# Kernel optimization log

Measured on AMD Instinct MI355X. Metric: run time of the kernel, lower is better.

## Reference

```python
import jax, jax.numpy as jnp
import numpy as np

N_EMBD = 1024
N_HEAD = 16
HEAD_DIM = N_EMBD // N_HEAD
EPS = 1e-5


def _gelu_tanh(x):
    c = jnp.sqrt(jnp.asarray(2.0 / jnp.pi, x.dtype))
    return 0.5 * x * (1.0 + jnp.tanh(c * (x + 0.044715 * x ** 3)))


def _layernorm(x, scale, shift):
    # torch.var defaults to unbiased (ddof=1) -- replicate exactly
    mean = jnp.mean(x, axis=-1, keepdims=True)
    var = jnp.var(x, axis=-1, keepdims=True, ddof=1)
    return (x - mean) / jnp.sqrt(var + EPS) * scale + shift


def setup_inputs() -> dict:
    key = jax.random.key(0)
    ks = jax.random.split(key, 8)
    d, h = N_EMBD, 4 * N_EMBD
    s = 0.02
    return {
        "x": jax.random.normal(ks[0], (2, 2048, d), jnp.float32),
        "ln1_scale": jnp.ones((d,), jnp.float32),
        "ln1_shift": jnp.zeros((d,), jnp.float32),
        "wq": jax.random.normal(ks[1], (d, d), jnp.float32) * s,
        "wk": jax.random.normal(ks[2], (d, d), jnp.float32) * s,
        "wv": jax.random.normal(ks[3], (d, d), jnp.float32) * s,
        "w_out": jax.random.normal(ks[4], (d, d), jnp.float32) * s,
        "b_out": jnp.zeros((d,), jnp.float32),
        "ln2_scale": jnp.ones((d,), jnp.float32),
        "ln2_shift": jnp.zeros((d,), jnp.float32),
        "w1": jax.random.normal(ks[5], (d, h), jnp.float32) * s,
        "b1": jnp.zeros((h,), jnp.float32),
        "w2": jax.random.normal(ks[6], (h, d), jnp.float32) * s,
        "b2": jnp.zeros((d,), jnp.float32),
    }


def reference(x, ln1_scale, ln1_shift, wq, wk, wv, w_out, b_out,
              ln2_scale, ln2_shift, w1, b1, w2, b2):
    B, S, D = x.shape
    out = _layernorm(x, ln1_scale, ln1_shift)

    # qkv projections (no bias), split heads: [B, H, S, hd]
    q = (out @ wq).reshape(B, S, N_HEAD, HEAD_DIM).transpose(0, 2, 1, 3)
    k = (out @ wk).reshape(B, S, N_HEAD, HEAD_DIM).transpose(0, 2, 1, 3)
    v = (out @ wv).reshape(B, S, N_HEAD, HEAD_DIM).transpose(0, 2, 1, 3)

    scores = jnp.einsum("bhqd,bhkd->bhqk", q, k)
    causal = jnp.triu(jnp.ones((S, S), bool), k=1)
    # original masks BEFORE scaling; -inf / sqrt(d) is still -inf
    scores = jnp.where(causal, -jnp.inf, scores)
    weights = jax.nn.softmax(scores / jnp.sqrt(jnp.asarray(HEAD_DIM, scores.dtype)), axis=-1)
    ctx = jnp.einsum("bhqk,bhkd->bqhd", weights, v).reshape(B, S, D)
    attn_out = ctx @ w_out + b_out

    out = attn_out + x  # dropout is identity (rate 0)
    shortcut = out
    out = _layernorm(out, ln2_scale, ln2_shift)
    out = _gelu_tanh(out @ w1 + b1) @ w2 + b2
    return out + shortcut
```

## Files before the change

### kernel.cpp

```cpp
#include <hip/hip_runtime.h>
#include <stdint.h>
#include <math.h>

using bf16x8 = __attribute__((ext_vector_type(8))) short;
using f32x4  = __attribute__((ext_vector_type(4))) float;

__device__ __forceinline__ uint16_t f2b(float f) {
    union { float f; uint32_t i; } v; v.f = f;
    uint32_t r = v.i + 0x7fffu + ((v.i >> 16) & 1u);
    return (uint16_t)(r >> 16);
}
__device__ __forceinline__ float b2f(uint16_t u) {
    union { uint32_t i; float f; } v; v.i = ((uint32_t)u) << 16; return v.f;
}

typedef const __attribute__((address_space(1))) void gvoid;
typedef __attribute__((address_space(3))) void svoid;

__global__ __launch_bounds__(256) void fill_zero(float* __restrict__ o, int n) {
    int i = (blockIdx.x * 256 + threadIdx.x) * 4;
    if (i < n) *(float4*)(o + i) = make_float4(0.f, 0.f, 0.f, 0.f);
}

__global__ __launch_bounds__(256) void transpose_qkvo(
    const float* __restrict__ wq, const float* __restrict__ wk,
    const float* __restrict__ wv, const float* __restrict__ wo,
    uint16_t* __restrict__ wqkvT, uint16_t* __restrict__ woT)
{
    const int D = 1024;
    int z = blockIdx.z;
    const float* W = (z == 0) ? wq : (z == 1) ? wk : (z == 2) ? wv : wo;
    uint16_t* Wt = (z < 3) ? (wqkvT + (size_t)z * D * D) : woT;
    __shared__ uint16_t t[32][33];
    int n0 = blockIdx.x * 32, k0 = blockIdx.y * 32;
    int tx = threadIdx.x, ty = threadIdx.y;
    #pragma unroll
    for (int i = ty; i < 32; i += 8)
        t[i][tx] = f2b(W[(size_t)(k0 + i) * D + (n0 + tx)]);
    __syncthreads();
    #pragma unroll
    for (int i = ty; i < 32; i += 8)
        Wt[(size_t)(n0 + i) * D + (k0 + tx)] = t[tx][i];
}

__global__ __launch_bounds__(256) void transpose_f2b(
    const float* __restrict__ W, uint16_t* __restrict__ Wt, int K, int N)
{
    __shared__ uint16_t t[32][33];
    int n0 = blockIdx.x * 32, k0 = blockIdx.y * 32;
    int tx = threadIdx.x, ty = threadIdx.y;
    #pragma unroll
    for (int i = ty; i < 32; i += 8)
        t[i][tx] = f2b(W[(size_t)(k0 + i) * N + (n0 + tx)]);
    __syncthreads();
    #pragma unroll
    for (int i = ty; i < 32; i += 8)
        Wt[(size_t)(n0 + i) * K + (k0 + tx)] = t[tx][i];
}

__global__ __launch_bounds__(256) void ln_kernel(
    const float* __restrict__ src, const float* __restrict__ scale,
    const float* __restrict__ shift, uint16_t* __restrict__ out)
{
    const int D = 1024;
    int row = blockIdx.x, t = threadIdx.x;
    float4 f = *((const float4*)(src + (size_t)row * D) + t);
    float v[4] = {f.x, f.y, f.z, f.w};
    float s1 = v[0] + v[1] + v[2] + v[3];
    float s2 = v[0]*v[0] + v[1]*v[1] + v[2]*v[2] + v[3]*v[3];
    #pragma unroll
    for (int off = 32; off; off >>= 1) {
        s1 += __shfl_xor(s1, off);
        s2 += __shfl_xor(s2, off);
    }
    __shared__ float red[2][4];
    __shared__ float stat[2];
    int wid = t >> 6, lane = t & 63;
    if (lane == 0) { red[0][wid] = s1; red[1][wid] = s2; }
    __syncthreads();
    if (t == 0) {
        float S1 = red[0][0] + red[0][1] + red[0][2] + red[0][3];
        float S2 = red[1][0] + red[1][1] + red[1][2] + red[1][3];
        float mean = S1 / (float)D;
        float var  = fmaxf((S2 - mean * S1) / (float)(D - 1), 0.f);
        stat[0] = mean; stat[1] = rsqrtf(var + 1e-5f);
    }
    __syncthreads();
    float mean = stat[0], rstd = stat[1];
    float4 sc = *((const float4*)scale + t);
    float4 sh = *((const float4*)shift + t);
    uint16_t o[4];
    o[0] = f2b((v[0] - mean) * rstd * sc.x + sh.x);
    o[1] = f2b((v[1] - mean) * rstd * sc.y + sh.y);
    o[2] = f2b((v[2] - mean) * rstd * sc.z + sh.z);
    o[3] = f2b((v[3] - mean) * rstd * sc.w + sh.w);
    uint2 st;
    st.x = (uint32_t)o[0] | ((uint32_t)o[1] << 16);
    st.y = (uint32_t)o[2] | ((uint32_t)o[3] << 16);
    *(uint2*)(out + (size_t)row * D + t * 4) = st;
}

__global__ __launch_bounds__(256) void combine2(
    float* __restrict__ dst, const float* __restrict__ part0,
    const float* __restrict__ resid, const float* __restrict__ bias)
{
    const int D = 1024;
    size_t o = (size_t)blockIdx.x * D + threadIdx.x * 4;
    float4 a = *(float4*)(dst + o);
    float4 b = *(const float4*)(part0 + o);
    float4 c = *(const float4*)(resid + o);
    float4 bv = *((const float4*)bias + threadIdx.x);
    a.x += b.x + c.x + bv.x;
    a.y += b.y + c.y + bv.y;
    a.z += b.z + c.z + bv.z;
    a.w += b.w + c.w + bv.w;
    *(float4*)(dst + o) = a;
}

__global__ __launch_bounds__(256) void combine2ln(
    float* __restrict__ res1, const float* __restrict__ part0,
    const float* __restrict__ x, const float* __restrict__ bo,
    const float* __restrict__ scale, const float* __restrict__ shift,
    uint16_t* __restrict__ out)
{
    const int D = 1024;
    int row = blockIdx.x, t = threadIdx.x;
    size_t o = (size_t)row * D + t * 4;
    float4 a = *(float4*)(res1 + o);
    float4 b = *(const float4*)(part0 + o);
    float4 c = *(const float4*)(x + o);
    float4 bv = *((const float4*)bo + t);
    float v[4] = {a.x + b.x + c.x + bv.x, a.y + b.y + c.y + bv.y,
                  a.z + b.z + c.z + bv.z, a.w + b.w + c.w + bv.w};
    *(float4*)(res1 + o) = make_float4(v[0], v[1], v[2], v[3]);

    float s1 = v[0] + v[1] + v[2] + v[3];
    float s2 = v[0]*v[0] + v[1]*v[1] + v[2]*v[2] + v[3]*v[3];
    #pragma unroll
    for (int off = 32; off; off >>= 1) {
        s1 += __shfl_xor(s1, off);
        s2 += __shfl_xor(s2, off);
    }
    __shared__ float red[2][4];
    __shared__ float stat[2];
    int wid = t >> 6, lane = t & 63;
    if (lane == 0) { red[0][wid] = s1; red[1][wid] = s2; }
    __syncthreads();
    if (t == 0) {
        float S1 = red[0][0] + red[0][1] + red[0][2] + red[0][3];
        float S2 = red[1][0] + red[1][1] + red[1][2] + red[1][3];
        float mean = S1 / (float)D;
        float var  = fmaxf((S2 - mean * S1) / (float)(D - 1), 0.f);
        stat[0] = mean; stat[1] = rsqrtf(var + 1e-5f);
    }
    __syncthreads();
    float mean = stat[0], rstd = stat[1];
    float4 sc = *((const float4*)scale + t);
    float4 sh = *((const float4*)shift + t);
    uint16_t ob[4];
    ob[0] = f2b((v[0] - mean) * rstd * sc.x + sh.x);
    ob[1] = f2b((v[1] - mean) * rstd * sc.y + sh.y);
    ob[2] = f2b((v[2] - mean) * rstd * sc.z + sh.z);
    ob[3] = f2b((v[3] - mean) * rstd * sc.w + sh.w);
    uint2 st;
    st.x = (uint32_t)ob[0] | ((uint32_t)ob[1] << 16);
    st.y = (uint32_t)ob[2] | ((uint32_t)ob[3] << 16);
    *(uint2*)(out + (size_t)row * D + t * 4) = st;
}

__device__ __forceinline__ void stage128(
    const uint16_t* __restrict__ A, const uint16_t* __restrict__ Bt,
    uint16_t* As, uint16_t* Bs,
    int m0, int n0, int lda, int kk, int w, int l)
{
    int srow = l >> 3;
    int sc = ((l & 7) ^ srow) << 3;
    #pragma unroll
    for (int p = 0; p < 4; ++p) {
        int rbase = w * 32 + p * 8;
        const uint16_t* ga = A  + (size_t)(m0 + rbase + srow) * lda + kk + sc;
        const uint16_t* gb = Bt + (size_t)(n0 + rbase + srow) * lda + kk + sc;
        __builtin_amdgcn_global_load_lds((gvoid*)ga, (svoid*)(As + rbase * 64), 16, 0, 0);
        __builtin_amdgcn_global_load_lds((gvoid*)gb, (svoid*)(Bs + rbase * 64), 16, 0, 0);
    }
}

__device__ __forceinline__ void comp128(
    const uint16_t* As, const uint16_t* Bs, f32x4 (&acc)[4][4],
    int mo, int no, int quad, int ln, int sw)
{
    #pragma unroll
    for (int s = 0; s < 2; ++s) {
        int cc = ((s * 64 + quad * 16) ^ sw) >> 1;
        bf16x8 af[4], bf[4];
        #pragma unroll
        for (int i = 0; i < 4; ++i)
            af[i] = *(const bf16x8*)(As + (mo + i * 16 + ln) * 64 + cc);
        #pragma unroll
        for (int i = 0; i < 4; ++i)
            bf[i] = *(const bf16x8*)(Bs + (no + i * 16 + ln) * 64 + cc);
        #pragma unroll
        for (int mi = 0; mi < 4; ++mi)
            #pragma unroll
            for (int ni = 0; ni < 4; ++ni)
                acc[mi][ni] = __builtin_amdgcn_mfma_f32_16x16x32_bf16(
                    af[mi], bf[ni], acc[mi][ni], 0, 0, 0);
    }
}

template <int EPI>
__global__ __launch_bounds__(256) void gemm128(
    const uint16_t* __restrict__ A, const uint16_t* __restrict__ Bt,
    const float* __restrict__ bias, const float* __restrict__ resid,
    void* __restrict__ outp, void* __restrict__ out2,
    int M, int N, int K, int lda)
{
    __shared__ __align__(16) uint16_t As0[128 * 64];
    __shared__ __align__(16) uint16_t As1[128 * 64];
    __shared__ __align__(16) uint16_t Bs0[128 * 64];
    __shared__ __align__(16) uint16_t Bs1[128 * 64];
    int tid = threadIdx.x;
    int w = tid >> 6, l = tid & 63;
    int quad = l >> 4, ln = l & 15;
    int sw = (ln & 7) << 4;

    int Nt = gridDim.x, Mt = gridDim.y;
    int L0 = blockIdx.y * Nt + blockIdx.x;
    int nb = Nt * Mt;
    int L = (L0 & 7) * (nb >> 3) + (L0 >> 3);
    const int GROUP = 8;
    int nig = GROUP * Nt;
    int gid = L / nig;
    int fm = gid * GROUP;
    int gsz = min(Mt - fm, GROUP);
    int rem = L - gid * nig;
    int pid_m = fm + rem % gsz;
    int pid_n = rem / gsz;
    int n0 = pid_n * 128, m0 = pid_m * 128;
    int kofs = (EPI == 5) ? blockIdx.z * K : 0;

    int mo = (w & 1) * 64, no = (w >> 1) * 64;

    f32x4 acc[4][4];
    #pragma unroll
    for (int mi = 0; mi < 4; ++mi)
        #pragma unroll
        for (int ni = 0; ni < 4; ++ni) acc[mi][ni] = (f32x4){0.f, 0.f, 0.f, 0.f};

    int nk = K >> 6;
    stage128(A, Bt, As0, Bs0, m0, n0, lda, kofs, w, l);
    __syncthreads();

    for (int t = 0; t + 2 <= nk; t += 2) {
        stage128(A, Bt, As1, Bs1, m0, n0, lda, kofs + (t + 1) * 64, w, l);
        comp128(As0, Bs0, acc, mo, no, quad, ln, sw);
        __syncthreads();
        if (t + 2 < nk)
            stage128(A, Bt, As0, Bs0, m0, n0, lda, kofs + (t + 2) * 64, w, l);
        comp128(As1, Bs1, acc, mo, no, quad, ln, sw);
        if (t + 2 < nk) __syncthreads();
    }

    float* pout = (EPI == 5) ? (blockIdx.z ? (float*)out2 : (float*)outp) : (float*)outp;

    #pragma unroll
    for (int ni = 0; ni < 4; ++ni) {
        int col = n0 + no + ni * 16 + ln;
        if (EPI == 4 && col >= 2048) {
            int hh = (col - 2048) >> 6, d = (col - 2048) & 63;
            #pragma unroll
            for (int mi = 0; mi < 4; ++mi) {
                int tok = m0 + mo + mi * 16 + quad * 4;
                int bat = tok >> 11, s = tok & 2047;
                uint16_t pk[4];
                #pragma unroll
                for (int r = 0; r < 4; ++r) pk[r] = f2b(acc[mi][ni][r]);
                uint2 st;
                st.x = (uint32_t)pk[0] | ((uint32_t)pk[1] << 16);
                st.y = (uint32_t)pk[2] | ((uint32_t)pk[3] << 16);
                *(uint2*)((uint16_t*)out2 +
                          ((size_t)(bat * 16 + hh) * 64 + d) * 2048 + s) = st;
            }
            continue;
        }
        float bv = (EPI == 1 || EPI == 2) ? bias[col] : 0.f;
        #pragma unroll
        for (int mi = 0; mi < 4; ++mi) {
            #pragma unroll
            for (int r = 0; r < 4; ++r) {
                int row = m0 + mo + mi * 16 + quad * 4 + r;
                float vacc = acc[mi][ni][r] + bv;
                if (EPI == 1) {
                    size_t idx = (size_t)row * N + col;
                    ((float*)outp)[idx] = vacc + resid[idx];
                } else if (EPI == 5) {
                    pout[(size_t)row * N + col] = vacc;
                } else if (EPI == 2) {
                    float x = vacc;
                    float u = 0.7978845608028654f * (x + 0.044715f * x * x * x);
                    float g = x / (1.f + __expf(-2.f * u));
                    ((uint16_t*)outp)[(size_t)row * N + col] = f2b(g);
                } else {
                    float vs = (col < 1024) ? vacc * 0.125f : vacc;
                    ((uint16_t*)outp)[(size_t)(col >> 10) * M * 1024 +
                                      (size_t)row * 1024 + (col & 1023)] = f2b(vs);
                }
            }
        }
    }
}

__device__ __forceinline__ void attn_tile(
    const uint16_t* __restrict__ Kl, const uint16_t* __restrict__ Vl,
    uint16_t* __restrict__ Pw,
    bf16x8 qf0, bf16x8 qf1,
    float* l_r, f32x4* o_acc,
    int qw, int kv0, bool diag, int quad, int ln)
{
    const int LW = 72;
    f32x4 sf[4];
    #pragma unroll
    for (int nt2 = 0; nt2 < 4; ++nt2) {
        const uint16_t* kp = Kl + (nt2 * 16 + ln) * LW + quad * 8;
        bf16x8 k0 = *(const bf16x8*)(kp);
        bf16x8 k1 = *(const bf16x8*)(kp + 32);
        f32x4 z = {0.f, 0.f, 0.f, 0.f};
        z = __builtin_amdgcn_mfma_f32_16x16x32_bf16(qf0, k0, z, 0, 0, 0);
        z = __builtin_amdgcn_mfma_f32_16x16x32_bf16(qf1, k1, z, 0, 0, 0);
        sf[nt2] = z;
    }
    #pragma unroll
    for (int r = 0; r < 4; ++r) {
        float ps = 0.f;
        if (diag) {
            int qrow = qw + quad * 4 + r;
            #pragma unroll
            for (int nt2 = 0; nt2 < 4; ++nt2) {
                int kv = kv0 + nt2 * 16 + ln;
                float pv = (kv <= qrow) ? __expf(sf[nt2][r]) : 0.f;
                sf[nt2][r] = pv;
                ps += pv;
            }
        } else {
            #pragma unroll
            for (int nt2 = 0; nt2 < 4; ++nt2) {
                float pv = __expf(sf[nt2][r]);
                sf[nt2][r] = pv;
                ps += pv;
            }
        }
        ps += __shfl_xor(ps, 1);
        ps += __shfl_xor(ps, 2);
        ps += __shfl_xor(ps, 4);
        ps += __shfl_xor(ps, 8);
        l_r[r] += ps;
    }
    #pragma unroll
    for (int nt2 = 0; nt2 < 4; ++nt2) {
        int gl = nt2 * 2 + (ln >> 3);
        int off = ln & 7;
        #pragma unroll
        for (int r = 0; r < 4; ++r) {
            int row = quad * 4 + r;
            int p = gl ^ ((quad << 1) ^ r);
            Pw[row * 64 + p * 8 + off] = f2b(sf[nt2][r]);
        }
    }
    int swl = ((ln >> 2) << 1) ^ (ln & 3);
    int g0 = quad ^ swl;
    int g1 = (quad + 4) ^ swl;
    bf16x8 p0 = *(const bf16x8*)(Pw + ln * 64 + g0 * 8);
    bf16x8 p1 = *(const bf16x8*)(Pw + ln * 64 + g1 * 8);
    #pragma unroll
    for (int dt = 0; dt < 4; ++dt) {
        const uint16_t* vp = Vl + (dt * 16 + ln) * LW + quad * 8;
        bf16x8 v0 = *(const bf16x8*)(vp);
        bf16x8 v1 = *(const bf16x8*)(vp + 32);
        o_acc[dt] = __builtin_amdgcn_mfma_f32_16x16x32_bf16(p0, v0, o_acc[dt], 0, 0, 0);
        o_acc[dt] = __builtin_amdgcn_mfma_f32_16x16x32_bf16(p1, v1, o_acc[dt], 0, 0, 0);
    }
}

__global__ __launch_bounds__(256) void attn_flash(
    const uint16_t* __restrict__ Q,
    const uint16_t* __restrict__ K,
    const uint16_t* __restrict__ Vt,
    uint16_t* __restrict__ O,
    int B, int S, int H)
{
    const int D = 1024;
    const int LW = 72;
    __shared__ uint16_t Kl[64 * 72];
    __shared__ uint16_t Vl[64 * 72];
    __shared__ uint16_t Pl[64 * 64];

    int tid = threadIdx.x;
    int w = tid >> 6, l = tid & 63;
    int quad = l >> 4, ln = l & 15;

    int NT = S / 64;
    int h = blockIdx.y, b = blockIdx.z;
    int qt = ((h >> 3) & 1) ? blockIdx.x : (NT - 1 - blockIdx.x);
    size_t rb = (size_t)b * S;

    int qw = qt * 64 + w * 16;

    const uint16_t* qp = Q + (rb + qw + ln) * D + h * 64 + quad * 8;
    bf16x8 q0 = *(const bf16x8*)(qp);
    bf16x8 q1 = *(const bf16x8*)(qp + 32);

    const uint16_t* Kbase = K + rb * D + h * 64;
    const uint16_t* Vbase = Vt + (size_t)(b * H + h) * 64 * S;
    uint16_t* Pw = Pl + w * 16 * 64;

    int sr0 = tid >> 3,         sc0 = (tid & 7) * 8;
    int sr1 = (256 + tid) >> 3, sc1 = ((256 + tid) & 7) * 8;

    float lr[4] = {0.f, 0.f, 0.f, 0.f};
    f32x4 oa[4];
    #pragma unroll
    for (int dt = 0; dt < 4; ++dt)
        oa[dt] = (f32x4){0.f, 0.f, 0.f, 0.f};

    uint4 kr0 = *(const uint4*)(Kbase + (size_t)sr0 * D + sc0);
    uint4 kr1 = *(const uint4*)(Kbase + (size_t)sr1 * D + sc1);
    uint4 vr0 = *(const uint4*)(Vbase + (size_t)sr0 * S + sc0);
    uint4 vr1 = *(const uint4*)(Vbase + (size_t)sr1 * S + sc1);

    for (int t = 0; t <= qt; ++t) {
        __syncthreads();
        *(uint4*)(Kl + sr0 * LW + sc0) = kr0;
        *(uint4*)(Kl + sr1 * LW + sc1) = kr1;
        *(uint4*)(Vl + sr0 * LW + sc0) = vr0;
        *(uint4*)(Vl + sr1 * LW + sc1) = vr1;
        __syncthreads();
        if (t < qt) {
            int kv1 = (t + 1) * 64;
            kr0 = *(const uint4*)(Kbase + (size_t)(kv1 + sr0) * D + sc0);
            kr1 = *(const uint4*)(Kbase + (size_t)(kv1 + sr1) * D + sc1);
            vr0 = *(const uint4*)(Vbase + (size_t)sr0 * S + kv1 + sc0);
            vr1 = *(const uint4*)(Vbase + (size_t)sr1 * S + kv1 + sc1);
        }
        attn_tile(Kl, Vl, Pw, q0, q1, lr, oa, qw, t * 64, t == qt, quad, ln);
    }

    #pragma unroll
    for (int r = 0; r < 4; ++r) {
        float inv = 1.f / lr[r];
        uint16_t* op = O + (rb + qw + quad * 4 + r) * D + h * 64 + ln;
        #pragma unroll
        for (int dt = 0; dt < 4; ++dt)
            op[dt * 16] = f2b(oa[dt][r] * inv);
    }
}

extern "C" void kernel_launch(void* const* d_in, const int* in_sizes, int n_in,
                              void* d_out, int out_size, void* d_ws, size_t ws_size,
                              hipStream_t stream)
{
    (void)in_sizes; (void)n_in;
    const int B = 2, S = 2048, D = 1024, H = 16, F = 4096;
    const int M = B * S;
    const size_t MB = 1u << 20;

    const float* x    = (const float*)d_in[0];
    const float* ln1s = (const float*)d_in[1];
    const float* ln1b = (const float*)d_in[2];
    const float* wq   = (const float*)d_in[3];
    const float* wk   = (const float*)d_in[4];
    const float* wv   = (const float*)d_in[5];
    const float* wo   = (const float*)d_in[6];
    const float* bo   = (const float*)d_in[7];
    const float* ln2s = (const float*)d_in[8];
    const float* ln2b = (const float*)d_in[9];
    const float* w1   = (const float*)d_in[10];
    const float* b1   = (const float*)d_in[11];
    const float* w2   = (const float*)d_in[12];
    const float* b2   = (const float*)d_in[13];

    if (ws_size < 56 * MB) {
        fill_zero<<<(out_size + 1023) / 1024, 256, 0, stream>>>((float*)d_out, out_size);
        return;
    }
    bool full = ws_size >= 72 * MB;

    char* base = (char*)d_ws;
    uint16_t* woT    = (uint16_t*)(base + 0 * MB);
    uint16_t* wqkvT  = (uint16_t*)(base + 2 * MB);
    uint16_t* ln1o   = (uint16_t*)(base + 8 * MB);
    uint16_t* qb     = (uint16_t*)(base + 16 * MB);
    uint16_t* vbT    = (uint16_t*)(base + 32 * MB);
    uint16_t* ctx    = (uint16_t*)(base + 40 * MB);
    uint16_t* kb     = (uint16_t*)(base + 24 * MB);
    uint16_t* w1T    = (uint16_t*)(base + 0 * MB);
    float*    res1   = (float*)   (base + (full ? 56 : 16) * MB);
    uint16_t* ln2o   = (uint16_t*)(base + (full ? 8 : 32) * MB);
    uint16_t* w2T    = (uint16_t*)(base + (full ? 16 : 40) * MB);
    uint16_t* h1     = (uint16_t*)(base + (full ? 24 : 48) * MB);
    float*    part0  = (float*)   (base + 0 * MB);
    float*    partP  = (float*)   (base + 8 * MB);

    dim3 tb(32, 8);
    transpose_qkvo<<<dim3(D / 32, D / 32, 4), tb, 0, stream>>>(
        wq, wk, wv, wo, wqkvT, woT);

    ln_kernel<<<M, 256, 0, stream>>>(x, ln1s, ln1b, ln1o);

    gemm128<4><<<dim3(3072 / 128, M / 128), 256, 0, stream>>>(
        ln1o, wqkvT, nullptr, nullptr, qb, vbT, M, 3072, D, D);

    attn_flash<<<dim3(S / 64, H, B), 256, 0, stream>>>(qb, kb, vbT, ctx, B, S, H);

    if (full) {
        gemm128<5><<<dim3(D / 128, M / 128, 2), 256, 0, stream>>>(
            ctx, woT, nullptr, nullptr, partP, res1, M, D, D / 2, D);
        combine2ln<<<M, 256, 0, stream>>>(res1, partP, x, bo, ln2s, ln2b, ln2o);
    } else {
        gemm128<1><<<dim3(D / 128, M / 128), 256, 0, stream>>>(
            ctx, woT, bo, x, res1, nullptr, M, D, D, D);
        ln_kernel<<<M, 256, 0, stream>>>(res1, ln2s, ln2b, ln2o);
    }

    transpose_f2b<<<dim3(F / 32, D / 32), tb, 0, stream>>>(w1, w1T, D, F);
    transpose_f2b<<<dim3(D / 32, F / 32), tb, 0, stream>>>(w2, w2T, F, D);

    if (full) {
        gemm128<2><<<dim3(F / 128, M / 128), 256, 0, stream>>>(
            ln2o, w1T, b1, nullptr, h1, nullptr, M, F, D, D);
        gemm128<5><<<dim3(D / 128, M / 128, 2), 256, 0, stream>>>(
            h1, w2T, nullptr, nullptr, part0, d_out, M, D, F / 2, F);
        combine2<<<M, 256, 0, stream>>>((float*)d_out, part0, res1, b2);
    } else {
        const int MH = M / 2;
        for (int half = 0; half < 2; ++half) {
            size_t ro = (size_t)half * MH;
            gemm128<2><<<dim3(F / 128, MH / 128), 256, 0, stream>>>(
                ln2o + ro * D, w1T, b1, nullptr, h1, nullptr, MH, F, D, D);
            gemm128<1><<<dim3(D / 128, MH / 128), 256, 0, stream>>>(
                h1, w2T, b2, res1 + ro * D, (float*)d_out + ro * D, nullptr, MH, D, F, F);
        }
    }
}
```

Measured before the change: 363.6 us.

## Add 256x256 eight-wave GEMM with ping-pong staging and use it for full path

Introduces a gemm256 kernel that uses 512 threads and a 256x256 output tile. It stages the K dimension in halves through global_load_lds into double-buffered LDS, interleaving the loads with four MFMA quadrants under barriers and setprio. It also remaps tile order for L2 locality. The QKV, out-projection, FC1 and FC2 GEMMs on the full path now use it. The aim is more data reuse per LDS byte and better overlap of memory with MFMA, at the cost of fewer blocks (small grids such as D/256 x M/256 x 2 = 64 blocks) and high register pressure.

```diff
diff --git a/kernel.cpp b/kernel.cpp
--- a/kernel.cpp
+++ b/kernel.cpp
@@ -4,6 +4,8 @@
 
 using bf16x8 = __attribute__((ext_vector_type(8))) short;
 using f32x4  = __attribute__((ext_vector_type(4))) float;
+
+#define MFMA16 __builtin_amdgcn_mfma_f32_16x16x32_bf16
 
 __device__ __forceinline__ uint16_t f2b(float f) {
     union { float f; uint32_t i; } v; v.f = f;
@@ -203,8 +205,7 @@
         for (int mi = 0; mi < 4; ++mi)
             #pragma unroll
             for (int ni = 0; ni < 4; ++ni)
-                acc[mi][ni] = __builtin_amdgcn_mfma_f32_16x16x32_bf16(
-                    af[mi], bf[ni], acc[mi][ni], 0, 0, 0);
+                acc[mi][ni] = MFMA16(af[mi], bf[ni], acc[mi][ni], 0, 0, 0);
     }
 }
 
@@ -310,6 +311,217 @@
     }
 }
 
+__device__ __forceinline__ void stage_half(
+    const uint16_t* __restrict__ Mat, uint16_t* lds,
+    int panel0, int lda, int kk, int w, int l)
+{
+    #pragma unroll
+    for (int i = 0; i < 2; ++i) {
+        int idx = i * 512 + w * 64 + l;
+        int row = idx >> 3;
+        int sc = ((idx & 7) ^ (row & 7)) << 3;
+        const uint16_t* g = Mat + (size_t)(panel0 + row) * lda + kk + sc;
+        __builtin_amdgcn_global_load_lds(
+            (gvoid*)g, (svoid*)(lds + (i * 512 + w * 64) * 8), 16, 0, 0);
+    }
+}
+
+template <int EPI>
+__global__ __launch_bounds__(512, 2) void gemm256(
+    const uint16_t* __restrict__ A, const uint16_t* __restrict__ Bt,
+    const float* __restrict__ bias, const float* __restrict__ resid,
+    void* __restrict__ outp, void* __restrict__ out2,
+    int M, int N, int K, int lda)
+{
+    __shared__ __align__(16) uint16_t AsL[32768];
+    __shared__ __align__(16) uint16_t BsL[32768];
+    int tid = threadIdx.x;
+    int w = tid >> 6, l = tid & 63;
+    int quad = l >> 4, ln = l & 15;
+    int wr = w >> 2, wc = w & 3;
+    int sw = (ln & 7) << 4;
+    int cc0 = ((quad * 16) ^ sw) >> 1;
+    int cc1 = ((64 + quad * 16) ^ sw) >> 1;
+
+    int Nt = gridDim.x, Mt = gridDim.y;
+    int L0 = blockIdx.y * Nt + blockIdx.x;
+    int nb = Nt * Mt;
+    int L = (L0 & 7) * (nb >> 3) + (L0 >> 3);
+    const int GROUP = 8;
+    int nig = GROUP * Nt;
+    int gid = L / nig;
+    int fm = gid * GROUP;
+    int gsz = min(Mt - fm, GROUP);
+    int rem = L - gid * nig;
+    int pid_m = fm + rem % gsz;
+    int pid_n = rem / gsz;
+    int n0 = pid_n * 256, m0 = pid_m * 256;
+    int kofs = (EPI == 5) ? blockIdx.z * K : 0;
+
+    f32x4 acc[8][4];
+    #pragma unroll
+    for (int mi = 0; mi < 8; ++mi)
+        #pragma unroll
+        for (int ni = 0; ni < 4; ++ni) acc[mi][ni] = (f32x4){0.f, 0.f, 0.f, 0.f};
+
+    int nk = K >> 6;
+
+    stage_half(Bt, BsL,         n0,       lda, kofs,      w, l);
+    stage_half(A,  AsL,         m0,       lda, kofs,      w, l);
+    stage_half(A,  AsL + 8192,  m0 + 128, lda, kofs,      w, l);
+    stage_half(Bt, BsL + 8192,  n0 + 128, lda, kofs,      w, l);
+    stage_half(Bt, BsL + 16384, n0,       lda, kofs + 64, w, l);
+    stage_half(A,  AsL + 16384, m0,       lda, kofs + 64, w, l);
+    asm volatile("s_waitcnt vmcnt(4)" ::: "memory");
+    __builtin_amdgcn_s_barrier();
+    __builtin_amdgcn_sched_barrier(0);
+
+    for (int t = 0; t < nk; ++t) {
+        int b = t & 1;
+        const uint16_t* Ar = AsL + b * 16384 + wr * 8192;
+        const uint16_t* Br = BsL + b * 16384 + (wc >> 1) * 8192 + (wc & 1) * 4096;
+        uint16_t* stA1 = AsL + (b ^ 1) * 16384 + 8192;
+        uint16_t* stB1 = BsL + (b ^ 1) * 16384 + 8192;
+        uint16_t* stA0 = AsL + b * 16384;
+        uint16_t* stB0 = BsL + b * 16384;
+        int kk1 = kofs + (t + 1) * 64;
+        int kk2 = kofs + (t + 2) * 64;
+        bool g1 = (t + 1) < nk, g2 = (t + 2) < nk;
+
+        bf16x8 af[4][2], bL[2][2], bH[2][2];
+
+        #pragma unroll
+        for (int mi = 0; mi < 4; ++mi) {
+            af[mi][0] = *(const bf16x8*)(Ar + (mi * 16 + ln) * 64 + cc0);
+            af[mi][1] = *(const bf16x8*)(Ar + (mi * 16 + ln) * 64 + cc1);
+        }
+        #pragma unroll
+        for (int ni = 0; ni < 2; ++ni) {
+            bL[ni][0] = *(const bf16x8*)(Br + (ni * 16 + ln) * 64 + cc0);
+            bL[ni][1] = *(const bf16x8*)(Br + (ni * 16 + ln) * 64 + cc1);
+        }
+        if (g1) stage_half(A, stA1, m0 + 128, lda, kk1, w, l);
+        __builtin_amdgcn_s_barrier();
+        __builtin_amdgcn_sched_barrier(0);
+        __builtin_amdgcn_s_setprio(1);
+        #pragma unroll
+        for (int mi = 0; mi < 4; ++mi)
+            #pragma unroll
+            for (int ni = 0; ni < 2; ++ni) {
+                acc[mi][ni] = MFMA16(af[mi][0], bL[ni][0], acc[mi][ni], 0, 0, 0);
+                acc[mi][ni] = MFMA16(af[mi][1], bL[ni][1], acc[mi][ni], 0, 0, 0);
+            }
+        __builtin_amdgcn_s_setprio(0);
+        __builtin_amdgcn_s_barrier();
+        __builtin_amdgcn_sched_barrier(0);
+
+        #pragma unroll
+        for (int ni = 0; ni < 2; ++ni) {
+            bH[ni][0] = *(const bf16x8*)(Br + ((ni + 2) * 16 + ln) * 64 + cc0);
+            bH[ni][1] = *(const bf16x8*)(Br + ((ni + 2) * 16 + ln) * 64 + cc1);
+        }
+        if (g1) stage_half(Bt, stB1, n0 + 128, lda, kk1, w, l);
+        __builtin_amdgcn_s_barrier();
+        __builtin_amdgcn_sched_barrier(0);
+        __builtin_amdgcn_s_setprio(1);
+        #pragma unroll
+        for (int mi = 0; mi < 4; ++mi)
+            #pragma unroll
+            for (int ni = 0; ni < 2; ++ni) {
+                acc[mi][ni + 2] = MFMA16(af[mi][0], bH[ni][0], acc[mi][ni + 2], 0, 0, 0);
+                acc[mi][ni + 2] = MFMA16(af[mi][1], bH[ni][1], acc[mi][ni + 2], 0, 0, 0);
+            }
+        __builtin_amdgcn_s_setprio(0);
+        __builtin_amdgcn_s_barrier();
+        __builtin_amdgcn_sched_barrier(0);
+
+        #pragma unroll
+        for (int mi = 0; mi < 4; ++mi) {
+            af[mi][0] = *(const bf16x8*)(Ar + ((mi + 4) * 16 + ln) * 64 + cc0);
+            af[mi][1] = *(const bf16x8*)(Ar + ((mi + 4) * 16 + ln) * 64 + cc1);
+        }
+        if (g2) stage_half(Bt, stB0, n0, lda, kk2, w, l);
+        __builtin_amdgcn_s_barrier();
+        __builtin_amdgcn_sched_barrier(0);
+        __builtin_amdgcn_s_setprio(1);
+        #pragma unroll
+        for (int mi = 0; mi < 4; ++mi)
+            #pragma unroll
+            for (int ni = 0; ni < 2; ++ni) {
+                acc[mi + 4][ni] = MFMA16(af[mi][0], bL[ni][0], acc[mi + 4][ni], 0, 0, 0);
+                acc[mi + 4][ni] = MFMA16(af[mi][1], bL[ni][1], acc[mi + 4][ni], 0, 0, 0);
+            }
+        __builtin_amdgcn_s_setprio(0);
+        __builtin_amdgcn_s_barrier();
+        __builtin_amdgcn_sched_barrier(0);
+
+        if (g2) {
+            stage_half(A, stA0, m0, lda, kk2, w, l);
+            asm volatile("s_waitcnt vmcnt(4)" ::: "memory");
+        } else if (g1) {
+            asm volatile("s_waitcnt vmcnt(0)" ::: "memory");
+        }
+        __builtin_amdgcn_s_barrier();
+        __builtin_amdgcn_sched_barrier(0);
+        __builtin_amdgcn_s_setprio(1);
+        #pragma unroll
+        for (int mi = 0; mi < 4; ++mi)
+            #pragma unroll
+            for (int ni = 0; ni < 2; ++ni) {
+                acc[mi + 4][ni + 2] = MFMA16(af[mi][0], bH[ni][0], acc[mi + 4][ni + 2], 0, 0, 0);
+                acc[mi + 4][ni + 2] = MFMA16(af[mi][1], bH[ni][1], acc[mi + 4][ni + 2], 0, 0, 0);
+            }
+        __builtin_amdgcn_s_setprio(0);
+        __builtin_amdgcn_s_barrier();
+        __builtin_amdgcn_sched_barrier(0);
+    }
+
+    float* pout = (EPI == 5) ? (blockIdx.z ? (float*)out2 : (float*)outp) : (float*)outp;
+
+    #pragma unroll
+    for (int ni = 0; ni < 4; ++ni) {
+        int col = n0 + wc * 64 + ni * 16 + ln;
+        if (EPI == 4 && col >= 2048) {
+            int hh = (col - 2048) >> 6, d = (col - 2048) & 63;
+            #pragma unroll
+            for (int mi = 0; mi < 8; ++mi) {
+                int tok = m0 + wr * 128 + mi * 16 + quad * 4;
+                int bat = tok >> 11, s = tok & 2047;
+                uint16_t pk[4];
+                #pragma unroll
+                for (int r = 0; r < 4; ++r) pk[r] = f2b(acc[mi][ni][r]);
+                uint2 st;
+                st.x = (uint32_t)pk[0] | ((uint32_t)pk[1] << 16);
+                st.y = (uint32_t)pk[2] | ((uint32_t)pk[3] << 16);
+                *(uint2*)((uint16_t*)out2 +
+                          ((size_t)(bat * 16 + hh) * 64 + d) * 2048 + s) = st;
+            }
+            continue;
+        }
+        float bv = (EPI == 2) ? bias[col] : 0.f;
+        #pragma unroll
+        for (int mi = 0; mi < 8; ++mi) {
+            #pragma unroll
+            for (int r = 0; r < 4; ++r) {
+                int row = m0 + wr * 128 + mi * 16 + quad * 4 + r;
+                float vacc = acc[mi][ni][r] + bv;
+                if (EPI == 5) {
+                    pout[(size_t)row * N + col] = vacc;
+                } else if (EPI == 2) {
+                    float x = vacc;
+                    float u = 0.7978845608028654f * (x + 0.044715f * x * x * x);
+                    float g = x / (1.f + __expf(-2.f * u));
+                    ((uint16_t*)outp)[(size_t)row * N + col] = f2b(g);
+                } else {
+                    float vs = (col < 1024) ? vacc * 0.125f : vacc;
+                    ((uint16_t*)outp)[(size_t)(col >> 10) * M * 1024 +
+                                      (size_t)row * 1024 + (col & 1023)] = f2b(vs);
+                }
+            }
+        }
+    }
+}
+
 __device__ __forceinline__ void attn_tile(
     const uint16_t* __restrict__ Kl, const uint16_t* __restrict__ Vl,
     uint16_t* __restrict__ Pw,
@@ -325,8 +537,8 @@
         bf16x8 k0 = *(const bf16x8*)(kp);
         bf16x8 k1 = *(const bf16x8*)(kp + 32);
         f32x4 z = {0.f, 0.f, 0.f, 0.f};
-        z = __builtin_amdgcn_mfma_f32_16x16x32_bf16(qf0, k0, z, 0, 0, 0);
-        z = __builtin_amdgcn_mfma_f32_16x16x32_bf16(qf1, k1, z, 0, 0, 0);
+        z = MFMA16(qf0, k0, z, 0, 0, 0);
+        z = MFMA16(qf1, k1, z, 0, 0, 0);
         sf[nt2] = z;
     }
     #pragma unroll
@@ -376,8 +588,8 @@
         const uint16_t* vp = Vl + (dt * 16 + ln) * LW + quad * 8;
         bf16x8 v0 = *(const bf16x8*)(vp);
         bf16x8 v1 = *(const bf16x8*)(vp + 32);
-        o_acc[dt] = __builtin_amdgcn_mfma_f32_16x16x32_bf16(p0, v0, o_acc[dt], 0, 0, 0);
-        o_acc[dt] = __builtin_amdgcn_mfma_f32_16x16x32_bf16(p1, v1, o_acc[dt], 0, 0, 0);
+        o_acc[dt] = MFMA16(p0, v0, o_acc[dt], 0, 0, 0);
+        o_acc[dt] = MFMA16(p1, v1, o_acc[dt], 0, 0, 0);
     }
 }
 
@@ -506,13 +718,18 @@
 
     ln_kernel<<<M, 256, 0, stream>>>(x, ln1s, ln1b, ln1o);
 
-    gemm128<4><<<dim3(3072 / 128, M / 128), 256, 0, stream>>>(
-        ln1o, wqkvT, nullptr, nullptr, qb, vbT, M, 3072, D, D);
+    if (full) {
+        gemm256<4><<<dim3(3072 / 256, M / 256), 512, 0, stream>>>(
+            ln1o, wqkvT, nullptr, nullptr, qb, vbT, M, 3072, D, D);
+    } else {
+        gemm128<4><<<dim3(3072 / 128, M / 128), 256, 0, stream>>>(
+            ln1o, wqkvT, nullptr, nullptr, qb, vbT, M, 3072, D, D);
+    }
 
     attn_flash<<<dim3(S / 64, H, B), 256, 0, stream>>>(qb, kb, vbT, ctx, B, S, H);
 
     if (full) {
-        gemm128<5><<<dim3(D / 128, M / 128, 2), 256, 0, stream>>>(
+        gemm256<5><<<dim3(D / 256, M / 256, 2), 512, 0, stream>>>(
             ctx, woT, nullptr, nullptr, partP, res1, M, D, D / 2, D);
         combine2ln<<<M, 256, 0, stream>>>(res1, partP, x, bo, ln2s, ln2b, ln2o);
     } else {
@@ -525,9 +742,9 @@
     transpose_f2b<<<dim3(D / 32, F / 32), tb, 0, stream>>>(w2, w2T, F, D);
 
     if (full) {
-        gemm128<2><<<dim3(F / 128, M / 128), 256, 0, stream>>>(
+        gemm256<2><<<dim3(F / 256, M / 256), 512, 0, stream>>>(
             ln2o, w1T, b1, nullptr, h1, nullptr, M, F, D, D);
-        gemm128<5><<<dim3(D / 128, M / 128, 2), 256, 0, stream>>>(
+        gemm256<5><<<dim3(D / 256, M / 256, 2), 512, 0, stream>>>(
             h1, w2T, nullptr, nullptr, part0, d_out, M, D, F / 2, F);
         combine2<<<M, 256, 0, stream>>>((float*)d_out, part0, res1, b2);
     } else {
```

Result: slower. 392.1 us (median of 3 runs) (+7.8%).
